# Optimization experiments

Measured on AMD Instinct MI355X. Metric: run time of the kernel, lower is better.

## Reference

```python
import jax, jax.numpy as jnp
import numpy as np

B, S, M, D, F, H = 1, 2048, 512, 1024, 4096, 16
DH = D // H
W = 256  # Longformer half-window: query attends to keys within +/-W global positions


def layer_norm(x, g, b, eps=1e-5):
    mu = jnp.mean(x, axis=-1, keepdims=True)
    var = jnp.var(x, axis=-1, keepdims=True)
    return (x - mu) * jax.lax.rsqrt(var + eps) * g + b


def rel_sinusoid(dists, d_model):
    # Transformer-XL sinusoidal embedding of (possibly negative) relative distances
    inv_freq = 1.0 / (10000.0 ** (jnp.arange(0, d_model, 2, dtype=jnp.float32) / d_model))
    ang = dists[:, None].astype(jnp.float32) * inv_freq[None, :]
    return jnp.concatenate([jnp.sin(ang), jnp.cos(ang)], axis=-1)  # [nR, D]


def setup_inputs() -> dict:
    key = jax.random.key(0)
    ks = jax.random.split(key, 18)
    sc = D ** -0.5
    inp = {
        "x": jax.random.normal(ks[0], (B, S, D), jnp.float32),
        "mem": jax.random.normal(ks[1], (B, M, D), jnp.float32),
        "Wq": jax.random.normal(ks[2], (D, D), jnp.float32) * sc,
        "Wk": jax.random.normal(ks[3], (D, D), jnp.float32) * sc,
        "Wv": jax.random.normal(ks[4], (D, D), jnp.float32) * sc,
        "Wo": jax.random.normal(ks[5], (D, D), jnp.float32) * sc,
        "Wr": jax.random.normal(ks[6], (D, D), jnp.float32) * sc,
        "u": jax.random.normal(ks[7], (H, DH), jnp.float32) * 0.02,
        "v": jax.random.normal(ks[8], (H, DH), jnp.float32) * 0.02,
        "ln1_g": jnp.ones((D,), jnp.float32),
        "ln1_b": jnp.zeros((D,), jnp.float32),
        "W1": jax.random.normal(ks[9], (D, F), jnp.float32) * sc,
        "b1": jnp.zeros((F,), jnp.float32),
        "W2": jax.random.normal(ks[10], (F, D), jnp.float32) * (F ** -0.5),
        "b2": jnp.zeros((D,), jnp.float32),
        "ln2_g": jnp.ones((D,), jnp.float32),
        "ln2_b": jnp.zeros((D,), jnp.float32),
    }
    return inp


def reference(x, mem, Wq, Wk, Wv, Wo, Wr, u, v, ln1_g, ln1_b, W1, b1, W2, b2, ln2_g, ln2_b):
    L = M + S  # key/value length after prepending XL memory
    kv = jnp.concatenate([mem, x], axis=1)  # [B, L, D]
    q = (x @ Wq).reshape(B, S, H, DH)
    k = (kv @ Wk).reshape(B, L, H, DH)
    vv = (kv @ Wv).reshape(B, L, H, DH)

    # relative distances: global query pos = M+i, key pos = j -> dist = M+i-j in [-(S-1), M+S-1]
    dists = jnp.arange(-(S - 1), M + S)  # [nR]
    R = (rel_sinusoid(dists, D) @ Wr).reshape(-1, H, DH)  # [nR, H, DH]

    AC = jnp.einsum("bqhd,blhd->bhql", q + u, k)          # content term
    BD_all = jnp.einsum("bqhd,rhd->bhqr", q + v, R)        # position term per distance
    qi = jnp.arange(S)[:, None]
    kj = jnp.arange(L)[None, :]
    dist = M + qi - kj                                       # [S, L]
    idx = dist + (S - 1)
    BD = jnp.take_along_axis(BD_all, jnp.broadcast_to(idx[None, None], (B, H, S, L)), axis=-1)

    scores = (AC + BD) * (DH ** -0.5)
    band = jnp.abs(dist) <= W                                # sliding-window (banded) mask
    scores = jnp.where(band[None, None], scores, -1e30)
    attn = jax.nn.softmax(scores, axis=-1)
    o = jnp.einsum("bhql,blhd->bqhd", attn, vv).reshape(B, S, D) @ Wo

    h = layer_norm(x + o, ln1_g, ln1_b)                      # residual + LN (dropout: eval mode)
    f = jax.nn.gelu(h @ W1 + b1) @ W2 + b2                   # FFN
    return layer_norm(h + f, ln2_g, ln2_b)
```

## Files before the change

kernel.cpp:

```cpp
#include <hip/hip_runtime.h>
#include <hip/hip_bf16.h>
#include <cstdint>

#define S_ 2048
#define M_ 512
#define L_ 2560
#define D_ 1024
#define F_ 4096
#define H_ 16
#define DH_ 64
#define W_ 256
#define NR_ 513
#define NRP_ 640

typedef unsigned int uint32;
typedef __attribute__((ext_vector_type(8))) short bf16x8;
typedef __attribute__((ext_vector_type(4))) float f32x4;

__device__ __forceinline__ ushort f2bf(float f) {
  uint32 u = __builtin_bit_cast(uint32, f);
  u += 0x7FFFu + ((u >> 16) & 1u);
  return (ushort)(u >> 16);
}
__device__ __forceinline__ float bf2f(ushort s) {
  uint32 u = ((uint32)s) << 16;
  return __builtin_bit_cast(float, u);
}
__device__ __forceinline__ ushort4 pack4(float4 vf) {
  ushort4 r;
  r.x = f2bf(vf.x); r.y = f2bf(vf.y); r.z = f2bf(vf.z); r.w = f2bf(vf.w);
  return r;
}
__device__ __forceinline__ float gelu_tanh(float x) {
  float t = 0.7978845608028654f * x * (1.f + 0.044715f * x * x);
  float e = __expf(2.f * t);
  float th = 1.f - 2.f / (e + 1.f);
  return 0.5f * x * (1.f + th);
}

__device__ __forceinline__ void gld_lds16(const ushort* g, ushort* l) {
  __builtin_amdgcn_global_load_lds((const __attribute__((address_space(1))) void*)g,
                                   (__attribute__((address_space(3))) void*)l, 16, 0, 0);
}

__device__ __forceinline__ void tr_tile(const float* __restrict__ in, ushort* __restrict__ out,
                                        int R, int C, int c0, int r0, int tx, int ty,
                                        float (*tile)[33]) {
#pragma unroll
  for (int i = 0; i < 4; i++)
    tile[ty + i * 8][tx] = in[(size_t)(r0 + ty + i * 8) * C + c0 + tx];
  __syncthreads();
#pragma unroll
  for (int i = 0; i < 4; i++)
    out[(size_t)(c0 + ty + i * 8) * R + r0 + tx] = f2bf(tile[tx][ty + i * 8]);
}

__global__ __launch_bounds__(256)
void prep_kernel(const float* __restrict__ x, const float* __restrict__ mem,
                 const float* __restrict__ Wq, const float* __restrict__ Wk,
                 const float* __restrict__ Wv, const float* __restrict__ Wo,
                 const float* __restrict__ Wr, const float* __restrict__ W1,
                 const float* __restrict__ W2,
                 ushort* __restrict__ WqT, ushort* __restrict__ WkT,
                 ushort* __restrict__ WvT, ushort* __restrict__ WoT,
                 ushort* __restrict__ WrT, ushort* __restrict__ W1T,
                 ushort* __restrict__ W2T,
                 ushort* __restrict__ kvb, ushort* __restrict__ remb) {
  __shared__ float tile[32][33];
  const int bid = blockIdx.x;
  const int tid = threadIdx.x;
  const int tx = tid & 31, ty = tid >> 5;

  if (bid < 5120) {
    const int which = bid >> 10, idx = bid & 1023;
    const float* ins[5] = {Wq, Wk, Wv, Wo, Wr};
    ushort* outs[5] = {WqT, WkT, WvT, WoT, WrT};
    tr_tile(ins[which], outs[which], 1024, 1024, (idx & 31) * 32, (idx >> 5) * 32, tx, ty, tile);
  } else if (bid < 9216) {
    const int idx = bid - 5120;
    tr_tile(W1, W1T, 1024, 4096, (idx % 128) * 32, (idx / 128) * 32, tx, ty, tile);
  } else if (bid < 13312) {
    const int idx = bid - 9216;
    tr_tile(W2, W2T, 4096, 1024, (idx & 31) * 32, (idx >> 5) * 32, tx, ty, tile);
  } else if (bid < 15872) {
    const int k = (bid - 13312) * 256 + tid;
    const int l = k >> 8, c = k & 255;
    const float4* src = (l < M_) ? (const float4*)(mem + (size_t)l * D_)
                                 : (const float4*)(x + (size_t)(l - M_) * D_);
    ((ushort4*)kvb)[k] = pack4(src[c]);
  } else {
    const int idx = (bid - 15872) * 256 + tid;
    const int r = idx >> 9, f = idx & 511;
    if (r < NR_) {
      float invf = expf(-(float)f * (9.210340371976184f / 512.0f));
      float ang = (float)(r - W_) * invf;
      remb[(size_t)r * D_ + f] = f2bf(sinf(ang));
      remb[(size_t)r * D_ + 512 + f] = f2bf(cosf(ang));
    } else if (r < NRP_) {
      remb[(size_t)r * D_ + f] = 0;
      remb[(size_t)r * D_ + 512 + f] = 0;
    }
  }
}

template <int EPI, int SPLITK>
__device__ __forceinline__
void gemm8p2_core(const ushort* __restrict__ A, const ushort* __restrict__ BT,
                  void* __restrict__ Cout, void* __restrict__ Cout2,
                  void* __restrict__ Cout3, void* __restrict__ Cout4,
                  const float* __restrict__ bias, int Msz, int Nsz, int Ksz, int Kstride,
                  int gx, int bid, int nwg, char* dyn) {
  const int tid = threadIdx.x;
  const int wave = tid >> 6, lane = tid & 63;
  const int wr = wave >> 2, wc = wave & 3;
  const int fr = lane & 15, gf = lane >> 4;
  const int sl = fr & 7;

  const int xcd = bid & 7, idx = bid >> 3;
  const int q = nwg >> 3, r8 = nwg & 7;
  const int swz = (xcd < r8 ? xcd * (q + 1) : r8 * (q + 1) + (xcd - r8) * q) + idx;
  const int gy = Msz / 128;
  const int bx = swz % gx;
  const int rest = swz / gx;
  const int by = rest % gy;
  const int bz = rest / gy;
  const int brow = by * 128, bcol = bx * 256;
  const int koff = (SPLITK > 1) ? bz * Ksz : 0;

  const int nt = Ksz >> 6;

  const int srow = tid >> 3;
  const int scol = ((tid & 7) ^ (srow & 7)) * 8;
  const ushort* Ab = A + (size_t)(brow + srow) * Kstride + koff + scol;
  const ushort* Bb = BT + (size_t)(bcol + srow) * Kstride + koff + scol;

  auto stageA = [&](int t, int qm) {
    gld_lds16(Ab + (size_t)(qm * 64) * Kstride + t * 64,
              (ushort*)(dyn + (t & 1) * 49152 + qm * 8192) + wave * 512);
  };
  auto stageB = [&](int t, int qn) {
#pragma unroll
    for (int j = 0; j < 2; j++)
      gld_lds16(Bb + (size_t)(qn * 128 + j * 64) * Kstride + t * 64,
                (ushort*)(dyn + (t & 1) * 49152 + 16384 + qn * 16384 + j * 8192) + wave * 512);
  };

  const int ar0 = (wr * 32 + fr) * 128;
  const int ar1 = (wr * 32 + 16 + fr) * 128;
  const int br0 = (wc * 32 + fr) * 128;
  const int br1 = (wc * 32 + 16 + fr) * 128;
  const int s0 = (gf ^ sl) * 16;
  const int s1 = ((4 + gf) ^ sl) * 16;

  f32x4 acc00[2][2] = {}, acc01[2][2] = {}, acc10[2][2] = {}, acc11[2][2] = {};

  stageA(0, 0); stageB(0, 0); stageB(0, 1); stageA(0, 1);
  stageA(1, 0); stageB(1, 0);
  asm volatile("s_waitcnt vmcnt(3)" ::: "memory");
  __builtin_amdgcn_s_barrier();
  __builtin_amdgcn_sched_barrier(0);

#define PH4(QM, QN, ACC, STAGES, WAITS)                                                 \
  {                                                                                     \
    const char* ab = dyn + cur * 49152 + (QM) * 8192;                                   \
    const char* bb = dyn + cur * 49152 + 16384 + (QN) * 16384;                          \
    bf16x8 a00 = *(const bf16x8*)(ab + ar0 + s0);                                       \
    bf16x8 a10 = *(const bf16x8*)(ab + ar1 + s0);                                       \
    bf16x8 a01 = *(const bf16x8*)(ab + ar0 + s1);                                       \
    bf16x8 a11 = *(const bf16x8*)(ab + ar1 + s1);                                       \
    bf16x8 b00 = *(const bf16x8*)(bb + br0 + s0);                                       \
    bf16x8 b10 = *(const bf16x8*)(bb + br1 + s0);                                       \
    bf16x8 b01 = *(const bf16x8*)(bb + br0 + s1);                                       \
    bf16x8 b11 = *(const bf16x8*)(bb + br1 + s1);                                       \
    STAGES;                                                                             \
    WAITS;                                                                              \
    __builtin_amdgcn_s_barrier();                                                       \
    asm volatile("s_waitcnt lgkmcnt(0)" ::: "memory");                                  \
    __builtin_amdgcn_sched_barrier(0);                                                  \
    __builtin_amdgcn_s_setprio(1);                                                      \
    ACC[0][0] = __builtin_amdgcn_mfma_f32_16x16x32_bf16(a00, b00, ACC[0][0], 0, 0, 0);  \
    ACC[0][1] = __builtin_amdgcn_mfma_f32_16x16x32_bf16(a00, b10, ACC[0][1], 0, 0, 0);  \
    ACC[1][0] = __builtin_amdgcn_mfma_f32_16x16x32_bf16(a10, b00, ACC[1][0], 0, 0, 0);  \
    ACC[1][1] = __builtin_amdgcn_mfma_f32_16x16x32_bf16(a10, b10, ACC[1][1], 0, 0, 0);  \
    ACC[0][0] = __builtin_amdgcn_mfma_f32_16x16x32_bf16(a01, b01, ACC[0][0], 0, 0, 0);  \
    ACC[0][1] = __builtin_amdgcn_mfma_f32_16x16x32_bf16(a01, b11, ACC[0][1], 0, 0, 0);  \
    ACC[1][0] = __builtin_amdgcn_mfma_f32_16x16x32_bf16(a11, b01, ACC[1][0], 0, 0, 0);  \
    ACC[1][1] = __builtin_amdgcn_mfma_f32_16x16x32_bf16(a11, b11, ACC[1][1], 0, 0, 0);  \
    __builtin_amdgcn_s_setprio(0);                                                      \
    __builtin_amdgcn_s_barrier();                                                       \
  }

  for (int t = 0; t < nt; t++) {
    const int cur = t & 1;
    PH4(0, 0, acc00, { if (t + 1 < nt) stageB(t + 1, 1); }, {});
    PH4(0, 1, acc01, { if (t + 1 < nt) stageA(t + 1, 1); }, {});
    PH4(1, 0, acc10, { if (t + 2 < nt) stageA(t + 2, 0); }, {});
    PH4(1, 1, acc11, { if (t + 2 < nt) stageB(t + 2, 0); },
        {
          if (t + 1 < nt) {
            if (t + 2 < nt) asm volatile("s_waitcnt vmcnt(3)" ::: "memory");
            else            asm volatile("s_waitcnt vmcnt(0)" ::: "memory");
          }
        });
  }
#undef PH4

  const int r4 = gf * 4;
  float* co = (float*)Cout;
  bool addb = (EPI == 3);
  if constexpr (SPLITK >= 2) {
    if (bz == 1) { co = (float*)Cout2; addb = false; }
  }
  if constexpr (SPLITK == 4) {
    if (bz == 2) { co = (float*)Cout3; addb = false; }
    if (bz == 3) { co = (float*)Cout4; addb = false; }
  }
  auto wrq = [&](const f32x4 (&ACC)[2][2], int QM, int QN) {
#pragma unroll
    for (int m = 0; m < 2; m++) {
#pragma unroll
      for (int n = 0; n < 2; n++) {
        const int col = bcol + QN * 128 + wc * 32 + n * 16 + fr;
        const int row0 = brow + QM * 64 + wr * 32 + m * 16 + r4;
        if constexpr (EPI == 5) {
          if (col < 1024) {
#pragma unroll
            for (int r = 0; r < 4; r++)
              ((ushort*)Cout)[(size_t)(row0 + r) * 1024 + col] = f2bf(ACC[m][n][r]);
          } else {
            ushort4 pk;
            pk.x = f2bf(ACC[m][n][0]); pk.y = f2bf(ACC[m][n][1]);
            pk.z = f2bf(ACC[m][n][2]); pk.w = f2bf(ACC[m][n][3]);
            *(ushort4*)((ushort*)Cout2 + (size_t)(col - 1024) * Msz + row0) = pk;
          }
        } else if constexpr (EPI == 0 || EPI == 2) {
#pragma unroll
          for (int r = 0; r < 4; r++) {
            float val = ACC[m][n][r];
            size_t o = (size_t)(row0 + r) * Nsz + col;
            if constexpr (EPI == 2) ((ushort*)Cout)[o] = f2bf(gelu_tanh(val + bias[col]));
            else ((ushort*)Cout)[o] = f2bf(val);
          }
        } else {
#pragma unroll
          for (int r = 0; r < 4; r++) {
            float val = ACC[m][n][r];
            co[(size_t)(row0 + r) * Nsz + col] = addb ? val + bias[col] : val;
          }
        }
      }
    }
  };
  wrq(acc00, 0, 0);
  wrq(acc01, 0, 1);
  wrq(acc10, 1, 0);
  wrq(acc11, 1, 1);
}

template <int EPI, int SPLITK>
__global__ __launch_bounds__(512)
void gemm8p2_kern(const ushort* __restrict__ A, const ushort* __restrict__ BT,
                  void* __restrict__ Cout, void* __restrict__ Cout2,
                  void* __restrict__ Cout3, void* __restrict__ Cout4,
                  const float* __restrict__ bias, int Msz, int Nsz, int Ksz, int Kstride,
                  int gx) {
  extern __shared__ __align__(16) char dyn[];
  gemm8p2_core<EPI, SPLITK>(A, BT, Cout, Cout2, Cout3, Cout4, bias,
                            Msz, Nsz, Ksz, Kstride, gx, blockIdx.x, gridDim.x, dyn);
}

__global__ __launch_bounds__(512)
void proj8p(const ushort* __restrict__ kvb, const ushort* __restrict__ WqT,
            const ushort* __restrict__ WkvT, const ushort* __restrict__ WrT,
            const ushort* __restrict__ remb,
            ushort* __restrict__ qb, ushort* __restrict__ kb,
            ushort* __restrict__ Vt, ushort* __restrict__ Rb) {
  extern __shared__ __align__(16) char dyn[];
  const int bid = blockIdx.x;
  if (bid < 64) {
    gemm8p2_core<0, 1>(kvb + 512 * 1024, WqT, qb, nullptr, nullptr, nullptr, nullptr,
                       2048, 1024, 1024, 1024, 4, bid, 64, dyn);
  } else if (bid < 224) {
    gemm8p2_core<5, 1>(kvb, WkvT, kb, Vt, nullptr, nullptr, nullptr,
                       2560, 2048, 1024, 1024, 8, bid - 64, 160, dyn);
  } else {
    gemm8p2_core<0, 1>(remb, WrT, Rb, nullptr, nullptr, nullptr, nullptr,
                       640, 1024, 1024, 1024, 4, bid - 224, 20, dyn);
  }
}

__global__ __launch_bounds__(256)
void attn_mfma4(const ushort* __restrict__ qb, const ushort* __restrict__ kb,
                const ushort* __restrict__ Vt, const ushort* __restrict__ Rb,
                const float* __restrict__ ubias, const float* __restrict__ vbias,
                ushort* __restrict__ attb) {
  const int bid = blockIdx.x;
  const int swz = (bid & 7) * 64 + (bid >> 3);
  const int h = swz >> 5;
  const int i0 = (swz & 31) * 64;
  const int tid = threadIdx.x;
  const int wave = tid >> 6, lane = tid & 63;
  const int g = lane >> 4, fr = lane & 15;
  const int hD = h * DH_;

  __shared__ __align__(16) ushort ring[4][16][64];
  __shared__ __align__(16) ushort Pl[4][16][40];

  const int qi = i0 + wave * 16 + fr;
  bf16x8 afu[2], afv[2];
#pragma unroll
  for (int kst = 0; kst < 2; kst++) {
    const int dof = kst * 32 + g * 8;
    bf16x8 qv = *(const bf16x8*)(qb + (size_t)qi * D_ + hD + dof);
    const float* up = ubias + hD + dof;
    const float* vp = vbias + hD + dof;
    bf16x8 au, av;
#pragma unroll
    for (int j = 0; j < 8; j++) {
      float q = bf2f((ushort)qv[j]);
      au[j] = (short)f2bf(q + up[j]);
      av[j] = (short)f2bf(q + vp[j]);
    }
    afu[kst] = au; afv[kst] = av;
  }

  const int jb = 256 + i0;
  const int smax = 2303 - i0;
  const int sbase = wave * 16;

  auto produce = [&](int r0, bf16x8 rf0, bf16x8 rf1) {
    f32x4 acc = {};
    __builtin_amdgcn_s_setprio(1);
    acc = __builtin_amdgcn_mfma_f32_16x16x32_bf16(afv[0], rf0, acc, 0, 0, 0);
    acc = __builtin_amdgcn_mfma_f32_16x16x32_bf16(afv[1], rf1, acc, 0, 0, 0);
    __builtin_amdgcn_s_setprio(0);
#pragma unroll
    for (int rr = 0; rr < 4; rr++)
      ring[wave][g * 4 + rr][(r0 + fr) & 63] = f2bf(acc[rr]);
  };
  auto loadRrow = [&](int row, bf16x8* out0, bf16x8* out1) {
    const int rc = row < 0 ? 0 : row;
    *out0 = *(const bf16x8*)(Rb + (size_t)rc * D_ + hD + g * 8);
    *out1 = *(const bf16x8*)(Rb + (size_t)rc * D_ + hD + 32 + g * 8);
  };
  auto loadK = [&](int ch, bf16x8 (&kp)[2][2]) {
#pragma unroll
    for (int half = 0; half < 2; half++) {
      const int sa = sbase + ch * 32 + half * 16 + fr;
      const int jc = (jb + sa < L_ - 1) ? (jb + sa) : (L_ - 1);
      kp[half][0] = *(const bf16x8*)(kb + (size_t)jc * 1024 + hD + g * 8);
      kp[half][1] = *(const bf16x8*)(kb + (size_t)jc * 1024 + hD + 32 + g * 8);
    }
  };
  auto loadV = [&](int ch, bf16x8 (&vp)[4]) {
    int kc = jb + sbase + ch * 32 + g * 8;
    if (kc > L_ - 8) kc = L_ - 8;
#pragma unroll
    for (int n = 0; n < 4; n++)
      vp[n] = *(const bf16x8*)(Vt + (size_t)(hD + n * 16 + fr) * L_ + kc);
  };

#pragma unroll
  for (int t = 0; t < 3; t++) {
    const int r0 = 480 + t * 16;
    bf16x8 rf0, rf1;
    loadRrow(r0 + fr, &rf0, &rf1);
    produce(r0, rf0, rf1);
  }

  float m4[4], l4[4];
  f32x4 oacc[4] = {};
#pragma unroll
  for (int rr = 0; rr < 4; rr++) { m4[rr] = -1e30f; l4[rr] = 0.f; }

  bf16x8 kA[2][2], vA[4], kB[2][2], vB[4];
  bf16x8 rP0a, rP0b, rP1a, rP1b;
  loadK(0, kA); loadV(0, vA);

  auto body = [&](int ch, bf16x8 (&kU)[2][2], bf16x8 (&vU)[4],
                  bf16x8 (&kP)[2][2], bf16x8 (&vP)[4], bool first) -> bool {
    const int c0 = sbase + ch * 32;
    if (c0 > smax) return false;
    if (!first) {
      const int r0 = 480 - ch * 32;
      produce(r0, rP0a, rP0b);
      produce(r0 + 16, rP1a, rP1b);
    }
    if (ch < 16) {
      const int r0n = 480 - (ch + 1) * 32;
      loadRrow(r0n + fr, &rP0a, &rP0b);
      loadRrow(r0n + 16 + fr, &rP1a, &rP1b);
      loadK(ch + 1, kP);
      loadV(ch + 1, vP);
    }
    f32x4 sc[2];
#pragma unroll
    for (int half = 0; half < 2; half++) {
      f32x4 acc = {};
      __builtin_amdgcn_s_setprio(1);
      acc = __builtin_amdgcn_mfma_f32_16x16x32_bf16(afu[0], kU[half][0], acc, 0, 0, 0);
      acc = __builtin_amdgcn_mfma_f32_16x16x32_bf16(afu[1], kU[half][1], acc, 0, 0, 0);
      __builtin_amdgcn_s_setprio(0);
      const int rb2 = 512 + g * 4 - (ch * 32 + half * 16 + fr);
      const int sa = c0 + half * 16 + fr;
#pragma unroll
      for (int rr = 0; rr < 4; rr++) {
        const int r = rb2 + rr;
        const float bd = bf2f(ring[wave][g * 4 + rr][r & 63]);
        const bool valid = ((unsigned)r <= 512u) && (sa <= smax);
        sc[half][rr] = valid ? (acc[rr] + bd) * 0.125f : -1e30f;
      }
    }
    if (first) {
      f32x4 cm;
#pragma unroll
      for (int rr = 0; rr < 4; rr++) cm[rr] = fmaxf(sc[0][rr], sc[1][rr]);
#pragma unroll
      for (int off = 8; off; off >>= 1)
#pragma unroll
        for (int rr = 0; rr < 4; rr++) cm[rr] = fmaxf(cm[rr], __shfl_xor(cm[rr], off));
#pragma unroll
      for (int rr = 0; rr < 4; rr++) m4[rr] = cm[rr];
    } else {
      bool rise = false;
#pragma unroll
      for (int rr = 0; rr < 4; rr++)
        rise |= (fmaxf(sc[0][rr], sc[1][rr]) > m4[rr] + 8.f);
      if (__any(rise)) {
        f32x4 cm;
#pragma unroll
        for (int rr = 0; rr < 4; rr++) cm[rr] = fmaxf(sc[0][rr], sc[1][rr]);
#pragma unroll
        for (int off = 8; off; off >>= 1)
#pragma unroll
          for (int rr = 0; rr < 4; rr++) cm[rr] = fmaxf(cm[rr], __shfl_xor(cm[rr], off));
#pragma unroll
        for (int rr = 0; rr < 4; rr++) {
          const float nm = fmaxf(m4[rr], cm[rr]);
          const float esc = __expf(m4[rr] - nm);
          m4[rr] = nm;
          l4[rr] *= esc;
#pragma unroll
          for (int n = 0; n < 4; n++) oacc[n][rr] *= esc;
        }
      }
    }
    f32x4 pA, pB;
#pragma unroll
    for (int rr = 0; rr < 4; rr++) {
      pA[rr] = __expf(sc[0][rr] - m4[rr]);
      pB[rr] = __expf(sc[1][rr] - m4[rr]);
      l4[rr] += pA[rr] + pB[rr];
    }
#pragma unroll
    for (int rr = 0; rr < 4; rr++) {
      Pl[wave][g * 4 + rr][fr]      = f2bf(pA[rr]);
      Pl[wave][g * 4 + rr][16 + fr] = f2bf(pB[rr]);
    }
    bf16x8 pf = *(const bf16x8*)&Pl[wave][fr][g * 8];
    __builtin_amdgcn_s_setprio(1);
#pragma unroll
    for (int n = 0; n < 4; n++)
      oacc[n] = __builtin_amdgcn_mfma_f32_16x16x32_bf16(pf, vU[n], oacc[n], 0, 0, 0);
    __builtin_amdgcn_s_setprio(0);
    return true;
  };

  bool cont = body(0, kA, vA, kB, vB, true);
  for (int ch = 1; ch < 17 && cont; ch += 2) {
    cont = body(ch, kB, vB, kA, vA, false);
    if (!cont || ch + 1 >= 17) break;
    cont = body(ch + 1, kA, vA, kB, vB, false);
  }

#pragma unroll
  for (int off = 8; off; off >>= 1)
#pragma unroll
    for (int rr = 0; rr < 4; rr++) l4[rr] += __shfl_xor(l4[rr], off);
#pragma unroll
  for (int rr = 0; rr < 4; rr++) {
    const float inv = 1.f / l4[rr];
    const size_t rowo = (size_t)(i0 + sbase + g * 4 + rr) * D_ + hD;
#pragma unroll
    for (int n = 0; n < 4; n++)
      attb[rowo + n * 16 + fr] = f2bf(oacc[n][rr] * inv);
  }
}

__global__ __launch_bounds__(256)
void ln_kernel(const float* __restrict__ a, const float* __restrict__ b,
               const float* __restrict__ c, const float* __restrict__ d,
               const float* __restrict__ e,
               const float* __restrict__ gamma, const float* __restrict__ beta,
               float* __restrict__ outf, ushort* __restrict__ outb) {
  const int row = blockIdx.x;
  const int tid = threadIdx.x;
  const int wave = tid >> 6, lane = tid & 63;
  float4 va = ((const float4*)(a + (size_t)row * D_))[tid];
  float4 vb4 = ((const float4*)(b + (size_t)row * D_))[tid];
  float4 xv;
  xv.x = va.x + vb4.x; xv.y = va.y + vb4.y; xv.z = va.z + vb4.z; xv.w = va.w + vb4.w;
  if (c) {
    float4 vc = ((const float4*)(c + (size_t)row * D_))[tid];
    xv.x += vc.x; xv.y += vc.y; xv.z += vc.z; xv.w += vc.w;
  }
  if (d) {
    float4 vd = ((const float4*)(d + (size_t)row * D_))[tid];
    xv.x += vd.x; xv.y += vd.y; xv.z += vd.z; xv.w += vd.w;
  }
  if (e) {
    float4 ve = ((const float4*)(e + (size_t)row * D_))[tid];
    xv.x += ve.x; xv.y += ve.y; xv.z += ve.z; xv.w += ve.w;
  }
  float s = xv.x + xv.y + xv.z + xv.w;
  float q = xv.x * xv.x + xv.y * xv.y + xv.z * xv.z + xv.w * xv.w;
#pragma unroll
  for (int off = 32; off; off >>= 1) { s += __shfl_xor(s, off); q += __shfl_xor(q, off); }
  __shared__ float red[8];
  if (lane == 0) { red[wave * 2] = s; red[wave * 2 + 1] = q; }
  __syncthreads();
  float ts = red[0] + red[2] + red[4] + red[6];
  float tq = red[1] + red[3] + red[5] + red[7];
  float mu = ts * (1.f / D_);
  float var = tq * (1.f / D_) - mu * mu;
  float rs = rsqrtf(var + 1e-5f);
  float4 g4 = ((const float4*)gamma)[tid];
  float4 be4 = ((const float4*)beta)[tid];
  float4 y;
  y.x = (xv.x - mu) * rs * g4.x + be4.x;
  y.y = (xv.y - mu) * rs * g4.y + be4.y;
  y.z = (xv.z - mu) * rs * g4.z + be4.z;
  y.w = (xv.w - mu) * rs * g4.w + be4.w;
  ((float4*)(outf + (size_t)row * D_))[tid] = y;
  if (outb) ((ushort4*)(outb + (size_t)row * D_))[tid] = pack4(y);
}

extern "C" void kernel_launch(void* const* d_in, const int* in_sizes, int n_in,
                              void* d_out, int out_size, void* d_ws, size_t ws_size,
                              hipStream_t stream) {
  const float* x    = (const float*)d_in[0];
  const float* mem  = (const float*)d_in[1];
  const float* Wq   = (const float*)d_in[2];
  const float* Wk   = (const float*)d_in[3];
  const float* Wv   = (const float*)d_in[4];
  const float* Wo   = (const float*)d_in[5];
  const float* Wr   = (const float*)d_in[6];
  const float* u    = (const float*)d_in[7];
  const float* v    = (const float*)d_in[8];
  const float* ln1g = (const float*)d_in[9];
  const float* ln1b = (const float*)d_in[10];
  const float* W1   = (const float*)d_in[11];
  const float* b1   = (const float*)d_in[12];
  const float* W2   = (const float*)d_in[13];
  const float* b2   = (const float*)d_in[14];
  const float* ln2g = (const float*)d_in[15];
  const float* ln2b = (const float*)d_in[16];
  float* out = (float*)d_out;

  char* ws = (char*)d_ws;
  size_t off = 0;
  auto take = [&](size_t n) { char* p = ws + off; off += (n + 255) & ~(size_t)255; return p; };

  ushort* WqT = (ushort*)take(2097152);
  ushort* WkT = (ushort*)take(2097152);
  ushort* WvT = (ushort*)take(2097152);
  ushort* WoT = (ushort*)take(2097152);
  ushort* WrT = (ushort*)take(2097152);
  ushort* W1T = (ushort*)take(8388608);
  ushort* W2T = (ushort*)take(8388608);

  char* regA = take(8388608);
  ushort* kvb  = (ushort*)regA;
  ushort* remb = (ushort*)(regA + 5242880);
  float*  fbuf = (float*)regA;

  char* regB = take(20185088);
  ushort* qb   = (ushort*)regB;
  ushort* kb   = (ushort*)(regB + 4194304);
  ushort* Vt   = (ushort*)(regB + 9437184);
  ushort* Rb   = (ushort*)(regB + 14680064);
  ushort* attb = (ushort*)(regB + 15990784);
  float*  o2b  = (float*)regB;
  ushort* g    = (ushort*)regB;

  float*  o2 = (float*)take(8388608);
  float*  h  = (float*)take(8388608);
  ushort* hb = (ushort*)take(4194304);

  float* p2 = (float*)WqT;
  float* p3 = (float*)W1T;

  prep_kernel<<<17152, 256, 0, stream>>>(x, mem, Wq, Wk, Wv, Wo, Wr, W1, W2,
                                         WqT, WkT, WvT, WoT, WrT, W1T, W2T, kvb, remb);

  proj8p<<<244, 512, 98304, stream>>>(kvb, WqT, WkT, WrT, remb, qb, kb, Vt, Rb);

  attn_mfma4<<<512, 256, 0, stream>>>(qb, kb, Vt, Rb, u, v, attb);

  gemm8p2_kern<1, 2><<<128, 512, 98304, stream>>>(attb, WoT, o2, o2b, nullptr, nullptr,
                                                  nullptr, 2048, 1024, 512, 1024, 4);
  ln_kernel<<<2048, 256, 0, stream>>>(x, o2, o2b, nullptr, nullptr, ln1g, ln1b, h, hb);

  gemm8p2_kern<2, 1><<<256, 512, 98304, stream>>>(hb, W1T, g, nullptr, nullptr, nullptr,
                                                  b1, 2048, 4096, 1024, 1024, 16);

  gemm8p2_kern<3, 4><<<256, 512, 98304, stream>>>(g, W2T, fbuf, o2, p2, p3,
                                                  b2, 2048, 1024, 1024, 4096, 4);
  ln_kernel<<<2048, 256, 0, stream>>>(h, fbuf, o2, p2, p3, ln2g, ln2b, out, nullptr);
}
```

Baseline: 189.3 us.

## Deepen the relative-position ring in attention so BD production runs one chunk ahead

The attention kernel's LDS ring holding the bf16 position-term (BD) values grows from 64 to 128 columns. The R-row loads and BD MFMA production now run one chunk ahead of use, and production moves after the P tile is written rather than at the start of each chunk. K/V prefetch is issued after the QK MFMAs, reordering the loads relative to the compute. The aim is to keep the BD dependency off the critical path of each chunk, at the cost of more LDS and more registers for the double-buffered R fragments.

```diff
diff --git a/kernel.cpp b/kernel.cpp
--- a/kernel.cpp
+++ b/kernel.cpp
@@ -290,7 +290,7 @@
 }
 
 __global__ __launch_bounds__(256)
-void attn_mfma4(const ushort* __restrict__ qb, const ushort* __restrict__ kb,
+void attn_mfma5(const ushort* __restrict__ qb, const ushort* __restrict__ kb,
                 const ushort* __restrict__ Vt, const ushort* __restrict__ Rb,
                 const float* __restrict__ ubias, const float* __restrict__ vbias,
                 ushort* __restrict__ attb) {
@@ -303,7 +303,7 @@
   const int g = lane >> 4, fr = lane & 15;
   const int hD = h * DH_;
 
-  __shared__ __align__(16) ushort ring[4][16][64];
+  __shared__ __align__(16) ushort ring[4][16][128];
   __shared__ __align__(16) ushort Pl[4][16][40];
 
   const int qi = i0 + wave * 16 + fr;
@@ -336,7 +336,7 @@
     __builtin_amdgcn_s_setprio(0);
 #pragma unroll
     for (int rr = 0; rr < 4; rr++)
-      ring[wave][g * 4 + rr][(r0 + fr) & 63] = f2bf(acc[rr]);
+      ring[wave][g * 4 + rr][(r0 + fr) & 127] = f2bf(acc[rr]);
   };
   auto loadRrow = [&](int row, bf16x8* out0, bf16x8* out1) {
     const int rc = row < 0 ? 0 : row;
@@ -374,25 +374,16 @@
   for (int rr = 0; rr < 4; rr++) { m4[rr] = -1e30f; l4[rr] = 0.f; }
 
   bf16x8 kA[2][2], vA[4], kB[2][2], vB[4];
-  bf16x8 rP0a, rP0b, rP1a, rP1b;
+  bf16x8 rA[4], rB[4];
+  loadRrow(448 + fr, &rA[0], &rA[1]);
+  loadRrow(464 + fr, &rA[2], &rA[3]);
   loadK(0, kA); loadV(0, vA);
 
   auto body = [&](int ch, bf16x8 (&kU)[2][2], bf16x8 (&vU)[4],
-                  bf16x8 (&kP)[2][2], bf16x8 (&vP)[4], bool first) -> bool {
+                  bf16x8 (&kP)[2][2], bf16x8 (&vP)[4],
+                  bf16x8 (&rU)[4], bf16x8 (&rP)[4], bool first) -> bool {
     const int c0 = sbase + ch * 32;
     if (c0 > smax) return false;
-    if (!first) {
-      const int r0 = 480 - ch * 32;
-      produce(r0, rP0a, rP0b);
-      produce(r0 + 16, rP1a, rP1b);
-    }
-    if (ch < 16) {
-      const int r0n = 480 - (ch + 1) * 32;
-      loadRrow(r0n + fr, &rP0a, &rP0b);
-      loadRrow(r0n + 16 + fr, &rP1a, &rP1b);
-      loadK(ch + 1, kP);
-      loadV(ch + 1, vP);
-    }
     f32x4 sc[2];
 #pragma unroll
     for (int half = 0; half < 2; half++) {
@@ -401,14 +392,26 @@
       acc = __builtin_amdgcn_mfma_f32_16x16x32_bf16(afu[0], kU[half][0], acc, 0, 0, 0);
       acc = __builtin_amdgcn_mfma_f32_16x16x32_bf16(afu[1], kU[half][1], acc, 0, 0, 0);
       __builtin_amdgcn_s_setprio(0);
+      sc[half] = acc;
+    }
+    if (ch < 16) {
+      loadK(ch + 1, kP);
+      loadV(ch + 1, vP);
+    }
+    if (ch < 15) {
+      loadRrow(416 - ch * 32 + fr, &rP[0], &rP[1]);
+      loadRrow(432 - ch * 32 + fr, &rP[2], &rP[3]);
+    }
+#pragma unroll
+    for (int half = 0; half < 2; half++) {
       const int rb2 = 512 + g * 4 - (ch * 32 + half * 16 + fr);
       const int sa = c0 + half * 16 + fr;
 #pragma unroll
       for (int rr = 0; rr < 4; rr++) {
         const int r = rb2 + rr;
-        const float bd = bf2f(ring[wave][g * 4 + rr][r & 63]);
+        const float bd = bf2f(ring[wave][g * 4 + rr][r & 127]);
         const bool valid = ((unsigned)r <= 512u) && (sa <= smax);
-        sc[half][rr] = valid ? (acc[rr] + bd) * 0.125f : -1e30f;
+        sc[half][rr] = valid ? (sc[half][rr] + bd) * 0.125f : -1e30f;
       }
     }
     if (first) {
@@ -458,6 +461,10 @@
       Pl[wave][g * 4 + rr][16 + fr] = f2bf(pB[rr]);
     }
     bf16x8 pf = *(const bf16x8*)&Pl[wave][fr][g * 8];
+    if (ch < 16) {
+      produce(448 - ch * 32, rU[0], rU[1]);
+      produce(464 - ch * 32, rU[2], rU[3]);
+    }
     __builtin_amdgcn_s_setprio(1);
 #pragma unroll
     for (int n = 0; n < 4; n++)
@@ -466,11 +473,11 @@
     return true;
   };
 
-  bool cont = body(0, kA, vA, kB, vB, true);
+  bool cont = body(0, kA, vA, kB, vB, rA, rB, true);
   for (int ch = 1; ch < 17 && cont; ch += 2) {
-    cont = body(ch, kB, vB, kA, vA, false);
+    cont = body(ch, kB, vB, kA, vA, rB, rA, false);
     if (!cont || ch + 1 >= 17) break;
-    cont = body(ch + 1, kA, vA, kB, vB, false);
+    cont = body(ch + 1, kA, vA, kB, vB, rA, rB, false);
   }
 
 #pragma unroll
@@ -595,7 +602,7 @@
 
   proj8p<<<244, 512, 98304, stream>>>(kvb, WqT, WkT, WrT, remb, qb, kb, Vt, Rb);
 
-  attn_mfma4<<<512, 256, 0, stream>>>(qb, kb, Vt, Rb, u, v, attb);
+  attn_mfma5<<<512, 256, 0, stream>>>(qb, kb, Vt, Rb, u, v, attb);
 
   gemm8p2_kern<1, 2><<<128, 512, 98304, stream>>>(attb, WoT, o2, o2b, nullptr, nullptr,
                                                   nullptr, 2048, 1024, 512, 1024, 4);
```

Result: no change. 187.9 us (-0.8%).
